# Optimization experiments

Measured on AMD Instinct MI355X. Metric: run time of the kernel, lower is better.

Reference implementation:

```python
import jax, jax.numpy as jnp
import numpy as np

N = 50000   # nodes
E = 800000  # edges (avg degree 16)
D = 128     # in_dim == hidden_dim


def setup_inputs() -> dict:
    key = jax.random.key(0)
    ks = jax.random.split(key, 8)
    x = jax.random.normal(ks[0], (N, D), dtype=jnp.float32)
    edge_index = jax.random.randint(ks[1], (2, E), 0, N, dtype=jnp.int32)
    s = 1.0 / np.sqrt(D)  # glorot-ish scale
    W0 = jax.random.normal(ks[2], (D, D), dtype=jnp.float32) * s
    W1 = jax.random.normal(ks[3], (D, D), dtype=jnp.float32) * s
    W2 = jax.random.normal(ks[4], (D, D), dtype=jnp.float32) * s
    b0 = jnp.zeros((D,), dtype=jnp.float32)
    b1 = jnp.zeros((D,), dtype=jnp.float32)
    b2 = jnp.zeros((D,), dtype=jnp.float32)
    return {"x": x, "edge_index": edge_index,
            "W0": W0, "b0": b0, "W1": W1, "b1": b1, "W2": W2, "b2": b2}


def reference(x, edge_index, W0, b0, W1, b1, W2, b2):
    # PyG GCNConv defaults: add self-loops, symmetric D^-1/2 (A+I) D^-1/2 norm,
    # linear transform first, bias added after aggregation.
    src, dst = edge_index[0], edge_index[1]
    loops = jnp.arange(N, dtype=src.dtype)
    src_f = jnp.concatenate([src, loops])  # [E+N]
    dst_f = jnp.concatenate([dst, loops])
    deg = jax.ops.segment_sum(jnp.ones_like(src_f, dtype=x.dtype), dst_f, num_segments=N)
    dinv = jnp.where(deg > 0, jax.lax.rsqrt(deg), 0.0)
    norm = dinv[src_f] * dinv[dst_f]  # [E+N]

    def gcn_layer(h, W, b):
        h = h @ W                                # [N, D]
        msg = h[src_f] * norm[:, None]           # [E+N, D] gather
        agg = jax.ops.segment_sum(msg, dst_f, num_segments=N)  # scatter-add
        return agg + b

    h = jax.nn.relu(gcn_layer(x, W0, b0))  # dropout p=0.0 is a no-op
    h = jax.nn.relu(gcn_layer(h, W1, b1))
    return gcn_layer(h, W2, b2)
```

## Files before the change

kernel.cpp:

```cpp
#include <hip/hip_runtime.h>
#include <hip/hip_fp16.h>

#define NN 50000
#define NPAD 50048
#define NE 800000
#define D 128
#define BPAD 136

typedef __attribute__((ext_vector_type(8))) short bf16x8;
typedef __attribute__((ext_vector_type(4))) float f32x4;

__device__ inline unsigned short f2bf(float f) {
    unsigned int b = __float_as_uint(f);
    return (unsigned short)((b + 0x7FFFu + ((b >> 16) & 1u)) >> 16);
}
__device__ inline float bf2f(unsigned short u) {
    return __uint_as_float(((unsigned int)u) << 16);
}


__global__ void k_degree(const int* __restrict__ dst, int* __restrict__ cnt,
                         int* __restrict__ rank) {
    int e = blockIdx.x * 256 + threadIdx.x;
    if (e < NE) {
        int d = dst[e];
        rank[e] = atomicAdd(&cnt[d], 1);
    }
}

__global__ void k_scan_block(const int* __restrict__ cnt, int* __restrict__ excl,
                             int* __restrict__ bsum) {
    __shared__ int sm[256];
    int t = threadIdx.x;
    int idx = blockIdx.x * 256 + t;
    int v = (idx < NN) ? cnt[idx] : 0;
    sm[t] = v;
    __syncthreads();
    for (int o = 1; o < 256; o <<= 1) {
        int u = (t >= o) ? sm[t - o] : 0;
        __syncthreads();
        sm[t] += u;
        __syncthreads();
    }
    if (idx < NN) excl[idx] = sm[t] - v;
    if (t == 255) bsum[blockIdx.x] = sm[255];
}

__global__ void k_scan_top(const int* __restrict__ bsum, int* __restrict__ boff) {
    __shared__ int sm[256];
    const int NB = (NN + 255) / 256;
    int t = threadIdx.x;
    int v = (t < NB) ? bsum[t] : 0;
    sm[t] = v;
    __syncthreads();
    for (int o = 1; o < 256; o <<= 1) {
        int u = (t >= o) ? sm[t - o] : 0;
        __syncthreads();
        sm[t] += u;
        __syncthreads();
    }
    if (t < NB) boff[t] = sm[t] - v;
}

__global__ void k_scan_add(int* __restrict__ rowptr, const int* __restrict__ boff,
                           const int* __restrict__ cnt, float* __restrict__ dinv) {
    int idx = blockIdx.x * 256 + threadIdx.x;
    if (idx < NN) {
        rowptr[idx] += boff[idx >> 8];
        dinv[idx] = rsqrtf((float)(cnt[idx] + 1));
    } else if (idx == NN) {
        rowptr[NN] = NE;
    }
}

__global__ void k_fill(const int* __restrict__ src, const int* __restrict__ dst,
                       const int* __restrict__ rowptr, const int* __restrict__ rank,
                       int* __restrict__ col) {
    int e = blockIdx.x * 256 + threadIdx.x;
    if (e < NE) {
        int d = dst[e];
        int pos = rowptr[d] + rank[e];
        __builtin_nontemporal_store(src[e], &col[pos]);
    }
}


__global__ void k_convW3(const float* __restrict__ W0, const float* __restrict__ W1,
                         const float* __restrict__ W2, unsigned short* __restrict__ Wh,
                         unsigned short* __restrict__ Wl) {
    int i = blockIdx.x * 256 + threadIdx.x;
    if (i >= 3 * D * D) return;
    int m = i / (D * D), r = i - m * (D * D);
    const float* W = (m == 0) ? W0 : ((m == 1) ? W1 : W2);
    int k = r >> 7, c = r & 127;
    float v = W[r];
    unsigned short h = f2bf(v);
    unsigned short l = f2bf(v - bf2f(h));
    Wh[(size_t)m * D * D + c * D + k] = h;
    Wl[(size_t)m * D * D + c * D + k] = l;
}


__device__ inline void gemm_store(f32x4 acc[2][4], const float* __restrict__ dinv,
                                  __half* __restrict__ C, int R0, int C0, int lr, int lg) {
    #pragma unroll
    for (int fr = 0; fr < 2; fr++) {
        int rb = R0 + fr * 16 + lg * 4;
        #pragma unroll
        for (int j = 0; j < 4; j++) {
            int r = rb + j;
            if (r < NN) {
                float s = dinv[r];
                #pragma unroll
                for (int fc = 0; fc < 4; fc++)
                    C[(size_t)r * D + C0 + fc * 16 + lr] =
                        __float2half_rn(acc[fr][fc][j] * s);
            }
        }
    }
}

__global__ __launch_bounds__(256, 3) void k_gemm_mfma(
        const unsigned short* __restrict__ Ah, const unsigned short* __restrict__ Al,
        const unsigned short* __restrict__ BhT, const unsigned short* __restrict__ BlT,
        const float* __restrict__ dinv, __half* __restrict__ C) {
    __shared__ short Bs_h[D * BPAD];
    int t = threadIdx.x;
    {
        int c = t >> 1;
        int k0 = (t & 1) * 64;
        const unsigned short* gh = BhT + c * D + k0;
        short* dh = Bs_h + c * BPAD + k0;
        #pragma unroll
        for (int i = 0; i < 8; i++)
            *(int4*)(dh + i * 8) = *(const int4*)(gh + i * 8);
    }
    __syncthreads();

    int w = t >> 6, ln = t & 63;
    int wr = w >> 1, wc = w & 1;
    int R0 = blockIdx.x * 64 + wr * 32;
    int C0 = wc * 64;
    int lr = ln & 15, lg = ln >> 4;

    f32x4 acc[2][4];
    #pragma unroll
    for (int a = 0; a < 2; a++)
        #pragma unroll
        for (int b = 0; b < 4; b++)
            acc[a][b] = (f32x4){0.f, 0.f, 0.f, 0.f};

    const unsigned short* Abh = Ah + (size_t)(R0 + lr) * D + lg * 8;
    const unsigned short* Abl = Al + (size_t)(R0 + lr) * D + lg * 8;

    #pragma unroll
    for (int ks = 0; ks < 4; ks++) {
        int ko = ks * 32;
        bf16x8 fa_h[2], fa_l[2], fb_h[4], fb_l[4];
        #pragma unroll
        for (int fr = 0; fr < 2; fr++) {
            fa_h[fr] = *(const bf16x8*)(Abh + fr * 16 * D + ko);
            fa_l[fr] = *(const bf16x8*)(Abl + fr * 16 * D + ko);
        }
        #pragma unroll
        for (int fc = 0; fc < 4; fc++) {
            int ccol = C0 + fc * 16 + lr;
            fb_h[fc] = *(const bf16x8*)(Bs_h + ccol * BPAD + ko + lg * 8);
            fb_l[fc] = *(const bf16x8*)(BlT + (size_t)ccol * D + ko + lg * 8);
        }
        #pragma unroll
        for (int fr = 0; fr < 2; fr++) {
            #pragma unroll
            for (int fc = 0; fc < 4; fc++) {
                acc[fr][fc] = __builtin_amdgcn_mfma_f32_16x16x32_bf16(
                    fa_h[fr], fb_h[fc], acc[fr][fc], 0, 0, 0);
                acc[fr][fc] = __builtin_amdgcn_mfma_f32_16x16x32_bf16(
                    fa_l[fr], fb_h[fc], acc[fr][fc], 0, 0, 0);
                acc[fr][fc] = __builtin_amdgcn_mfma_f32_16x16x32_bf16(
                    fa_h[fr], fb_l[fc], acc[fr][fc], 0, 0, 0);
            }
        }
    }
    gemm_store(acc, dinv, C, R0, C0, lr, lg);
}

__global__ __launch_bounds__(256, 2) void k_gemm_mfma_x(
        const float* __restrict__ X,
        const unsigned short* __restrict__ BhT, const unsigned short* __restrict__ BlT,
        const float* __restrict__ dinv, __half* __restrict__ C) {
    __shared__ short Bs_h[D * BPAD];
    int t = threadIdx.x;
    {
        int c = t >> 1;
        int k0 = (t & 1) * 64;
        const unsigned short* gh = BhT + c * D + k0;
        short* dh = Bs_h + c * BPAD + k0;
        #pragma unroll
        for (int i = 0; i < 8; i++)
            *(int4*)(dh + i * 8) = *(const int4*)(gh + i * 8);
    }
    __syncthreads();

    int w = t >> 6, ln = t & 63;
    int wr = w >> 1, wc = w & 1;
    int R0 = blockIdx.x * 64 + wr * 32;
    int C0 = wc * 64;
    int lr = ln & 15, lg = ln >> 4;

    f32x4 acc[2][4];
    #pragma unroll
    for (int a = 0; a < 2; a++)
        #pragma unroll
        for (int b = 0; b < 4; b++)
            acc[a][b] = (f32x4){0.f, 0.f, 0.f, 0.f};

    const float* Ab = X + (size_t)(R0 + lr) * D + lg * 8;

    #pragma unroll
    for (int ks = 0; ks < 4; ks++) {
        int ko = ks * 32;
        bf16x8 fa_h[2], fa_l[2], fb_h[4], fb_l[4];
        #pragma unroll
        for (int fr = 0; fr < 2; fr++) {
            float4 p0 = *(const float4*)(Ab + fr * 16 * D + ko);
            float4 p1 = *(const float4*)(Ab + fr * 16 * D + ko + 4);
            float vv[8] = {p0.x, p0.y, p0.z, p0.w, p1.x, p1.y, p1.z, p1.w};
            #pragma unroll
            for (int j = 0; j < 8; j++) {
                unsigned short h = f2bf(vv[j]);
                fa_h[fr][j] = (short)h;
                fa_l[fr][j] = (short)f2bf(vv[j] - bf2f(h));
            }
        }
        #pragma unroll
        for (int fc = 0; fc < 4; fc++) {
            int ccol = C0 + fc * 16 + lr;
            fb_h[fc] = *(const bf16x8*)(Bs_h + ccol * BPAD + ko + lg * 8);
            fb_l[fc] = *(const bf16x8*)(BlT + (size_t)ccol * D + ko + lg * 8);
        }
        #pragma unroll
        for (int fr = 0; fr < 2; fr++) {
            #pragma unroll
            for (int fc = 0; fc < 4; fc++) {
                acc[fr][fc] = __builtin_amdgcn_mfma_f32_16x16x32_bf16(
                    fa_h[fr], fb_h[fc], acc[fr][fc], 0, 0, 0);
                acc[fr][fc] = __builtin_amdgcn_mfma_f32_16x16x32_bf16(
                    fa_l[fr], fb_h[fc], acc[fr][fc], 0, 0, 0);
                acc[fr][fc] = __builtin_amdgcn_mfma_f32_16x16x32_bf16(
                    fa_h[fr], fb_l[fc], acc[fr][fc], 0, 0, 0);
            }
        }
    }
    gemm_store(acc, dinv, C, R0, C0, lr, lg);
}


__global__ __launch_bounds__(256) void k_agg(const __half* __restrict__ T,
                                             const int* __restrict__ rowptr,
                                             const int* __restrict__ col,
                                             const float* __restrict__ dinv,
                                             const float* __restrict__ bias,
                                             unsigned short* __restrict__ Oh,
                                             unsigned short* __restrict__ Ol,
                                             float* __restrict__ Of, int mode) {
    int i = blockIdx.x * 8 + (threadIdx.x >> 5);
    int sl = threadIdx.x & 31;
    int f = sl * 4;
    float di = dinv[i];
    float2 raw = *(const float2*)(T + (size_t)i * D + f);
    __half2 s0 = *(__half2*)&raw.x, s1 = *(__half2*)&raw.y;
    float2 g0 = __half22float2(s0), g1 = __half22float2(s1);
    float a0 = g0.x, a1 = g0.y, a2 = g1.x, a3 = g1.y;

    int e = rowptr[i], r1 = rowptr[i + 1];
    for (; e + 8 <= r1; e += 8) {
        float2 rv[8];
        #pragma unroll
        for (int u = 0; u < 8; u++) {
            int s = col[e + u];
            rv[u] = *(const float2*)(T + (size_t)s * D + f);
        }
        #pragma unroll
        for (int u = 0; u < 8; u++) {
            __half2 x0 = *(__half2*)&rv[u].x, x1 = *(__half2*)&rv[u].y;
            float2 q0 = __half22float2(x0), q1 = __half22float2(x1);
            a0 += q0.x; a1 += q0.y; a2 += q1.x; a3 += q1.y;
        }
    }
    for (; e + 4 <= r1; e += 4) {
        float2 rv[4];
        #pragma unroll
        for (int u = 0; u < 4; u++) {
            int s = col[e + u];
            rv[u] = *(const float2*)(T + (size_t)s * D + f);
        }
        #pragma unroll
        for (int u = 0; u < 4; u++) {
            __half2 x0 = *(__half2*)&rv[u].x, x1 = *(__half2*)&rv[u].y;
            float2 q0 = __half22float2(x0), q1 = __half22float2(x1);
            a0 += q0.x; a1 += q0.y; a2 += q1.x; a3 += q1.y;
        }
    }
    for (; e < r1; e++) {
        int s = col[e];
        float2 rv = *(const float2*)(T + (size_t)s * D + f);
        __half2 x0 = *(__half2*)&rv.x, x1 = *(__half2*)&rv.y;
        float2 q0 = __half22float2(x0), q1 = __half22float2(x1);
        a0 += q0.x; a1 += q0.y; a2 += q1.x; a3 += q1.y;
    }

    float4 bv = *(const float4*)(bias + f);
    a0 = a0 * di + bv.x;
    a1 = a1 * di + bv.y;
    a2 = a2 * di + bv.z;
    a3 = a3 * di + bv.w;
    if (mode) {
        a0 = fmaxf(a0, 0.f); a1 = fmaxf(a1, 0.f);
        a2 = fmaxf(a2, 0.f); a3 = fmaxf(a3, 0.f);
        unsigned short h0 = f2bf(a0), h1 = f2bf(a1), h2 = f2bf(a2), h3 = f2bf(a3);
        unsigned short l0 = f2bf(a0 - bf2f(h0)), l1 = f2bf(a1 - bf2f(h1));
        unsigned short l2 = f2bf(a2 - bf2f(h2)), l3 = f2bf(a3 - bf2f(h3));
        uint2 ph = make_uint2((unsigned)h0 | ((unsigned)h1 << 16),
                              (unsigned)h2 | ((unsigned)h3 << 16));
        uint2 pl = make_uint2((unsigned)l0 | ((unsigned)l1 << 16),
                              (unsigned)l2 | ((unsigned)l3 << 16));
        *(uint2*)(Oh + (size_t)i * D + f) = ph;
        *(uint2*)(Ol + (size_t)i * D + f) = pl;
    } else {
        *(float4*)(Of + (size_t)i * D + f) = make_float4(a0, a1, a2, a3);
    }
}


extern "C" void kernel_launch(void* const* d_in, const int* in_sizes, int n_in,
                              void* d_out, int out_size, void* d_ws, size_t ws_size,
                              hipStream_t stream) {
    const float* x  = (const float*)d_in[0];
    const int* edge = (const int*)d_in[1];
    const float* W0 = (const float*)d_in[2];
    const float* b0 = (const float*)d_in[3];
    const float* W1 = (const float*)d_in[4];
    const float* b1 = (const float*)d_in[5];
    const float* W2 = (const float*)d_in[6];
    const float* b2 = (const float*)d_in[7];
    const int* src = edge;
    const int* dst = edge + NE;
    float* out = (float*)d_out;

    char* ws = (char*)d_ws;
    size_t off = 0;
    auto alloc = [&](size_t bytes) {
        void* p = ws + off;
        off += (bytes + 255) & ~(size_t)255;
        return p;
    };
    int*   cnt    = (int*)alloc(NN * 4);
    int*   rowptr = (int*)alloc((NN + 1) * 4);
    float* dinv   = (float*)alloc(NN * 4);
    int*   bsum   = (int*)alloc(256 * 4);
    int*   boff   = (int*)alloc(256 * 4);
    int*   rank   = (int*)alloc((size_t)NE * 4);
    int*   col    = (int*)alloc((size_t)NE * 4);
    unsigned short* Wh = (unsigned short*)alloc(3 * D * D * 2);
    unsigned short* Wl = (unsigned short*)alloc(3 * D * D * 2);
    unsigned short* Xh = (unsigned short*)alloc((size_t)NPAD * D * 2);
    unsigned short* Xl = (unsigned short*)alloc((size_t)NPAD * D * 2);
    __half* T = (__half*)alloc((size_t)NPAD * D * 2);

    hipMemsetAsync(cnt, 0, NN * 4, stream);

    k_degree<<<(NE + 255) / 256, 256, 0, stream>>>(dst, cnt, rank);
    k_scan_block<<<(NN + 255) / 256, 256, 0, stream>>>(cnt, rowptr, bsum);
    k_scan_top<<<1, 256, 0, stream>>>(bsum, boff);
    k_scan_add<<<(NN + 256) / 256, 256, 0, stream>>>(rowptr, boff, cnt, dinv);
    k_fill<<<(NE + 255) / 256, 256, 0, stream>>>(src, dst, rowptr, rank, col);
    k_convW3<<<(3 * D * D + 255) / 256, 256, 0, stream>>>(W0, W1, W2, Wh, Wl);

    const int ggrid = (NN + 63) / 64;
    const int agrid = NN / 8;

    k_gemm_mfma_x<<<ggrid, 256, 0, stream>>>(x, Wh, Wl, dinv, T);
    k_agg<<<agrid, 256, 0, stream>>>(T, rowptr, col, dinv, b0, Xh, Xl, out, 1);
    k_gemm_mfma<<<ggrid, 256, 0, stream>>>(Xh, Xl, Wh + D * D, Wl + D * D, dinv, T);
    k_agg<<<agrid, 256, 0, stream>>>(T, rowptr, col, dinv, b1, Xh, Xl, out, 1);
    k_gemm_mfma<<<ggrid, 256, 0, stream>>>(Xh, Xl, Wh + 2 * D * D, Wl + 2 * D * D, dinv, T);
    k_agg<<<agrid, 256, 0, stream>>>(T, rowptr, col, dinv, b2, Xh, Xl, out, 0);
}
```

Baseline: 244.0 us.

## Fuse aggregation with next-layer GEMM via shared-memory split-bf16 tile

Each middle layer now runs one kernel: a block aggregates 64 nodes, applies bias and ReLU, splits the result into bf16 hi/lo parts in shared memory, then runs the MFMA GEMM straight from LDS. This removes the global write and re-read of the Xh/Xl intermediates and two kernel launches. In exchange, each block's gather phase and GEMM phase run back to back without overlap. The weights now come from global memory instead of LDS, and there are fewer, larger blocks for the irregular gather.

```diff
diff --git a/kernel.cpp b/kernel.cpp
--- a/kernel.cpp
+++ b/kernel.cpp
@@ -6,6 +6,7 @@
 #define NE 800000
 #define D 128
 #define BPAD 136
+#define APAD 136
 
 typedef __attribute__((ext_vector_type(8))) short bf16x8;
 typedef __attribute__((ext_vector_type(4))) float f32x4;
@@ -120,69 +121,6 @@
     }
 }
 
-__global__ __launch_bounds__(256, 3) void k_gemm_mfma(
-        const unsigned short* __restrict__ Ah, const unsigned short* __restrict__ Al,
-        const unsigned short* __restrict__ BhT, const unsigned short* __restrict__ BlT,
-        const float* __restrict__ dinv, __half* __restrict__ C) {
-    __shared__ short Bs_h[D * BPAD];
-    int t = threadIdx.x;
-    {
-        int c = t >> 1;
-        int k0 = (t & 1) * 64;
-        const unsigned short* gh = BhT + c * D + k0;
-        short* dh = Bs_h + c * BPAD + k0;
-        #pragma unroll
-        for (int i = 0; i < 8; i++)
-            *(int4*)(dh + i * 8) = *(const int4*)(gh + i * 8);
-    }
-    __syncthreads();
-
-    int w = t >> 6, ln = t & 63;
-    int wr = w >> 1, wc = w & 1;
-    int R0 = blockIdx.x * 64 + wr * 32;
-    int C0 = wc * 64;
-    int lr = ln & 15, lg = ln >> 4;
-
-    f32x4 acc[2][4];
-    #pragma unroll
-    for (int a = 0; a < 2; a++)
-        #pragma unroll
-        for (int b = 0; b < 4; b++)
-            acc[a][b] = (f32x4){0.f, 0.f, 0.f, 0.f};
-
-    const unsigned short* Abh = Ah + (size_t)(R0 + lr) * D + lg * 8;
-    const unsigned short* Abl = Al + (size_t)(R0 + lr) * D + lg * 8;
-
-    #pragma unroll
-    for (int ks = 0; ks < 4; ks++) {
-        int ko = ks * 32;
-        bf16x8 fa_h[2], fa_l[2], fb_h[4], fb_l[4];
-        #pragma unroll
-        for (int fr = 0; fr < 2; fr++) {
-            fa_h[fr] = *(const bf16x8*)(Abh + fr * 16 * D + ko);
-            fa_l[fr] = *(const bf16x8*)(Abl + fr * 16 * D + ko);
-        }
-        #pragma unroll
-        for (int fc = 0; fc < 4; fc++) {
-            int ccol = C0 + fc * 16 + lr;
-            fb_h[fc] = *(const bf16x8*)(Bs_h + ccol * BPAD + ko + lg * 8);
-            fb_l[fc] = *(const bf16x8*)(BlT + (size_t)ccol * D + ko + lg * 8);
-        }
-        #pragma unroll
-        for (int fr = 0; fr < 2; fr++) {
-            #pragma unroll
-            for (int fc = 0; fc < 4; fc++) {
-                acc[fr][fc] = __builtin_amdgcn_mfma_f32_16x16x32_bf16(
-                    fa_h[fr], fb_h[fc], acc[fr][fc], 0, 0, 0);
-                acc[fr][fc] = __builtin_amdgcn_mfma_f32_16x16x32_bf16(
-                    fa_l[fr], fb_h[fc], acc[fr][fc], 0, 0, 0);
-                acc[fr][fc] = __builtin_amdgcn_mfma_f32_16x16x32_bf16(
-                    fa_h[fr], fb_l[fc], acc[fr][fc], 0, 0, 0);
-            }
-        }
-    }
-    gemm_store(acc, dinv, C, R0, C0, lr, lg);
-}
 
 __global__ __launch_bounds__(256, 2) void k_gemm_mfma_x(
         const float* __restrict__ X,
@@ -255,14 +193,124 @@
 }
 
 
-__global__ __launch_bounds__(256) void k_agg(const __half* __restrict__ T,
-                                             const int* __restrict__ rowptr,
-                                             const int* __restrict__ col,
-                                             const float* __restrict__ dinv,
-                                             const float* __restrict__ bias,
-                                             unsigned short* __restrict__ Oh,
-                                             unsigned short* __restrict__ Ol,
-                                             float* __restrict__ Of, int mode) {
+__global__ __launch_bounds__(256, 3) void k_agg_gemm(
+        const __half* __restrict__ T_in,
+        const int* __restrict__ rowptr, const int* __restrict__ col,
+        const float* __restrict__ dinv, const float* __restrict__ bias,
+        const unsigned short* __restrict__ BhT, const unsigned short* __restrict__ BlT,
+        __half* __restrict__ T_out) {
+    __shared__ short Ah_s[64 * APAD];
+    __shared__ short Al_s[64 * APAD];
+    int t = threadIdx.x;
+    int base = blockIdx.x * 64;
+    int g = t >> 5, sl = t & 31;
+    int f = sl * 4;
+
+    float4 bv = *(const float4*)(bias + f);
+
+    for (int j = 0; j < 8; j++) {
+        int n = g + j * 8;
+        int i = base + n;
+        float a0 = 0.f, a1 = 0.f, a2 = 0.f, a3 = 0.f;
+        if (i < NN) {
+            float di = dinv[i];
+            float2 raw = *(const float2*)(T_in + (size_t)i * D + f);
+            {
+                __half2 x0 = *(__half2*)&raw.x, x1 = *(__half2*)&raw.y;
+                float2 q0 = __half22float2(x0), q1 = __half22float2(x1);
+                a0 = q0.x; a1 = q0.y; a2 = q1.x; a3 = q1.y;
+            }
+            int e = rowptr[i], r1 = rowptr[i + 1];
+            for (; e + 8 <= r1; e += 8) {
+                float2 rv[8];
+                #pragma unroll
+                for (int u = 0; u < 8; u++) {
+                    int s = col[e + u];
+                    rv[u] = *(const float2*)(T_in + (size_t)s * D + f);
+                }
+                #pragma unroll
+                for (int u = 0; u < 8; u++) {
+                    __half2 x0 = *(__half2*)&rv[u].x, x1 = *(__half2*)&rv[u].y;
+                    float2 q0 = __half22float2(x0), q1 = __half22float2(x1);
+                    a0 += q0.x; a1 += q0.y; a2 += q1.x; a3 += q1.y;
+                }
+            }
+            for (; e < r1; e++) {
+                int s = col[e];
+                float2 rv = *(const float2*)(T_in + (size_t)s * D + f);
+                __half2 x0 = *(__half2*)&rv.x, x1 = *(__half2*)&rv.y;
+                float2 q0 = __half22float2(x0), q1 = __half22float2(x1);
+                a0 += q0.x; a1 += q0.y; a2 += q1.x; a3 += q1.y;
+            }
+            a0 = fmaxf(a0 * di + bv.x, 0.f);
+            a1 = fmaxf(a1 * di + bv.y, 0.f);
+            a2 = fmaxf(a2 * di + bv.z, 0.f);
+            a3 = fmaxf(a3 * di + bv.w, 0.f);
+        }
+        unsigned short h0 = f2bf(a0), h1 = f2bf(a1), h2 = f2bf(a2), h3 = f2bf(a3);
+        unsigned short l0 = f2bf(a0 - bf2f(h0)), l1 = f2bf(a1 - bf2f(h1));
+        unsigned short l2 = f2bf(a2 - bf2f(h2)), l3 = f2bf(a3 - bf2f(h3));
+        *(uint2*)(Ah_s + n * APAD + f) = make_uint2(
+            (unsigned)h0 | ((unsigned)h1 << 16), (unsigned)h2 | ((unsigned)h3 << 16));
+        *(uint2*)(Al_s + n * APAD + f) = make_uint2(
+            (unsigned)l0 | ((unsigned)l1 << 16), (unsigned)l2 | ((unsigned)l3 << 16));
+    }
+    __syncthreads();
+
+    int w = t >> 6, ln = t & 63;
+    int wr = w >> 1, wc = w & 1;
+    int R0 = base + wr * 32;
+    int C0 = wc * 64;
+    int lr = ln & 15, lg = ln >> 4;
+
+    f32x4 acc[2][4];
+    #pragma unroll
+    for (int a = 0; a < 2; a++)
+        #pragma unroll
+        for (int b = 0; b < 4; b++)
+            acc[a][b] = (f32x4){0.f, 0.f, 0.f, 0.f};
+
+    const short* As_h = Ah_s + (wr * 32 + lr) * APAD + lg * 8;
+    const short* As_l = Al_s + (wr * 32 + lr) * APAD + lg * 8;
+
+    #pragma unroll
+    for (int ks = 0; ks < 4; ks++) {
+        int ko = ks * 32;
+        bf16x8 fa_h[2], fa_l[2], fb_h[4], fb_l[4];
+        #pragma unroll
+        for (int fr = 0; fr < 2; fr++) {
+            fa_h[fr] = *(const bf16x8*)(As_h + fr * 16 * APAD + ko);
+            fa_l[fr] = *(const bf16x8*)(As_l + fr * 16 * APAD + ko);
+        }
+        #pragma unroll
+        for (int fc = 0; fc < 4; fc++) {
+            int ccol = C0 + fc * 16 + lr;
+            fb_h[fc] = *(const bf16x8*)(BhT + (size_t)ccol * D + ko + lg * 8);
+            fb_l[fc] = *(const bf16x8*)(BlT + (size_t)ccol * D + ko + lg * 8);
+        }
+        #pragma unroll
+        for (int fr = 0; fr < 2; fr++) {
+            #pragma unroll
+            for (int fc = 0; fc < 4; fc++) {
+                acc[fr][fc] = __builtin_amdgcn_mfma_f32_16x16x32_bf16(
+                    fa_h[fr], fb_h[fc], acc[fr][fc], 0, 0, 0);
+                acc[fr][fc] = __builtin_amdgcn_mfma_f32_16x16x32_bf16(
+                    fa_l[fr], fb_h[fc], acc[fr][fc], 0, 0, 0);
+                acc[fr][fc] = __builtin_amdgcn_mfma_f32_16x16x32_bf16(
+                    fa_h[fr], fb_l[fc], acc[fr][fc], 0, 0, 0);
+            }
+        }
+    }
+    gemm_store(acc, dinv, T_out, R0, C0, lr, lg);
+}
+
+
+__global__ __launch_bounds__(256) void k_agg_out(const __half* __restrict__ T,
+                                                 const int* __restrict__ rowptr,
+                                                 const int* __restrict__ col,
+                                                 const float* __restrict__ dinv,
+                                                 const float* __restrict__ bias,
+                                                 float* __restrict__ Of) {
     int i = blockIdx.x * 8 + (threadIdx.x >> 5);
     int sl = threadIdx.x & 31;
     int f = sl * 4;
@@ -287,20 +335,6 @@
             a0 += q0.x; a1 += q0.y; a2 += q1.x; a3 += q1.y;
         }
     }
-    for (; e + 4 <= r1; e += 4) {
-        float2 rv[4];
-        #pragma unroll
-        for (int u = 0; u < 4; u++) {
-            int s = col[e + u];
-            rv[u] = *(const float2*)(T + (size_t)s * D + f);
-        }
-        #pragma unroll
-        for (int u = 0; u < 4; u++) {
-            __half2 x0 = *(__half2*)&rv[u].x, x1 = *(__half2*)&rv[u].y;
-            float2 q0 = __half22float2(x0), q1 = __half22float2(x1);
-            a0 += q0.x; a1 += q0.y; a2 += q1.x; a3 += q1.y;
-        }
-    }
     for (; e < r1; e++) {
         int s = col[e];
         float2 rv = *(const float2*)(T + (size_t)s * D + f);
@@ -310,25 +344,8 @@
     }
 
     float4 bv = *(const float4*)(bias + f);
-    a0 = a0 * di + bv.x;
-    a1 = a1 * di + bv.y;
-    a2 = a2 * di + bv.z;
-    a3 = a3 * di + bv.w;
-    if (mode) {
-        a0 = fmaxf(a0, 0.f); a1 = fmaxf(a1, 0.f);
-        a2 = fmaxf(a2, 0.f); a3 = fmaxf(a3, 0.f);
-        unsigned short h0 = f2bf(a0), h1 = f2bf(a1), h2 = f2bf(a2), h3 = f2bf(a3);
-        unsigned short l0 = f2bf(a0 - bf2f(h0)), l1 = f2bf(a1 - bf2f(h1));
-        unsigned short l2 = f2bf(a2 - bf2f(h2)), l3 = f2bf(a3 - bf2f(h3));
-        uint2 ph = make_uint2((unsigned)h0 | ((unsigned)h1 << 16),
-                              (unsigned)h2 | ((unsigned)h3 << 16));
-        uint2 pl = make_uint2((unsigned)l0 | ((unsigned)l1 << 16),
-                              (unsigned)l2 | ((unsigned)l3 << 16));
-        *(uint2*)(Oh + (size_t)i * D + f) = ph;
-        *(uint2*)(Ol + (size_t)i * D + f) = pl;
-    } else {
-        *(float4*)(Of + (size_t)i * D + f) = make_float4(a0, a1, a2, a3);
-    }
+    *(float4*)(Of + (size_t)i * D + f) = make_float4(
+        a0 * di + bv.x, a1 * di + bv.y, a2 * di + bv.z, a3 * di + bv.w);
 }
 
 
@@ -363,9 +380,8 @@
     int*   col    = (int*)alloc((size_t)NE * 4);
     unsigned short* Wh = (unsigned short*)alloc(3 * D * D * 2);
     unsigned short* Wl = (unsigned short*)alloc(3 * D * D * 2);
-    unsigned short* Xh = (unsigned short*)alloc((size_t)NPAD * D * 2);
-    unsigned short* Xl = (unsigned short*)alloc((size_t)NPAD * D * 2);
-    __half* T = (__half*)alloc((size_t)NPAD * D * 2);
+    __half* Ta = (__half*)alloc((size_t)NPAD * D * 2);
+    __half* Tb = (__half*)alloc((size_t)NPAD * D * 2);
 
     hipMemsetAsync(cnt, 0, NN * 4, stream);
 
@@ -379,10 +395,10 @@
     const int ggrid = (NN + 63) / 64;
     const int agrid = NN / 8;
 
-    k_gemm_mfma_x<<<ggrid, 256, 0, stream>>>(x, Wh, Wl, dinv, T);
-    k_agg<<<agrid, 256, 0, stream>>>(T, rowptr, col, dinv, b0, Xh, Xl, out, 1);
-    k_gemm_mfma<<<ggrid, 256, 0, stream>>>(Xh, Xl, Wh + D * D, Wl + D * D, dinv, T);
-    k_agg<<<agrid, 256, 0, stream>>>(T, rowptr, col, dinv, b1, Xh, Xl, out, 1);
-    k_gemm_mfma<<<ggrid, 256, 0, stream>>>(Xh, Xl, Wh + 2 * D * D, Wl + 2 * D * D, dinv, T);
-    k_agg<<<agrid, 256, 0, stream>>>(T, rowptr, col, dinv, b2, Xh, Xl, out, 0);
-}
+    k_gemm_mfma_x<<<ggrid, 256, 0, stream>>>(x, Wh, Wl, dinv, Ta);
+    k_agg_gemm<<<ggrid, 256, 0, stream>>>(Ta, rowptr, col, dinv, b0,
+                                          Wh + D * D, Wl + D * D, Tb);
+    k_agg_gemm<<<ggrid, 256, 0, stream>>>(Tb, rowptr, col, dinv, b1,
+                                          Wh + 2 * D * D, Wl + 2 * D * D, Ta);
+    k_agg_out<<<agrid, 256, 0, stream>>>(Ta, rowptr, col, dinv, b2, out);
+}
```

After: 266.1 us. +9.1%, slower.

## Store hidden activations in fp16 and widen aggregation loads to 16 bytes

Applied to the files above, without the earlier changes.

The aggregation kernel now writes one fp16 hidden buffer instead of separate bf16 hi/lo planes, and the GEMM splits each fp16 value into bf16 hi/lo in registers. This halves activation write and read traffic between layers. Aggregation now uses 16 lanes per node with 8 features each, so every gather is a 16-byte load, and the 4-edge tail loop is dropped. The degree kernel also writes rank with a nontemporal store. Storing hidden activations in fp16 loses a little precision compared with the bf16 hi/lo pair.

```diff
diff --git a/kernel.cpp b/kernel.cpp
--- a/kernel.cpp
+++ b/kernel.cpp
@@ -24,7 +24,8 @@
     int e = blockIdx.x * 256 + threadIdx.x;
     if (e < NE) {
         int d = dst[e];
-        rank[e] = atomicAdd(&cnt[d], 1);
+        int r = atomicAdd(&cnt[d], 1);
+        __builtin_nontemporal_store(r, &rank[e]);
     }
 }
 
@@ -120,69 +121,6 @@
     }
 }
 
-__global__ __launch_bounds__(256, 3) void k_gemm_mfma(
-        const unsigned short* __restrict__ Ah, const unsigned short* __restrict__ Al,
-        const unsigned short* __restrict__ BhT, const unsigned short* __restrict__ BlT,
-        const float* __restrict__ dinv, __half* __restrict__ C) {
-    __shared__ short Bs_h[D * BPAD];
-    int t = threadIdx.x;
-    {
-        int c = t >> 1;
-        int k0 = (t & 1) * 64;
-        const unsigned short* gh = BhT + c * D + k0;
-        short* dh = Bs_h + c * BPAD + k0;
-        #pragma unroll
-        for (int i = 0; i < 8; i++)
-            *(int4*)(dh + i * 8) = *(const int4*)(gh + i * 8);
-    }
-    __syncthreads();
-
-    int w = t >> 6, ln = t & 63;
-    int wr = w >> 1, wc = w & 1;
-    int R0 = blockIdx.x * 64 + wr * 32;
-    int C0 = wc * 64;
-    int lr = ln & 15, lg = ln >> 4;
-
-    f32x4 acc[2][4];
-    #pragma unroll
-    for (int a = 0; a < 2; a++)
-        #pragma unroll
-        for (int b = 0; b < 4; b++)
-            acc[a][b] = (f32x4){0.f, 0.f, 0.f, 0.f};
-
-    const unsigned short* Abh = Ah + (size_t)(R0 + lr) * D + lg * 8;
-    const unsigned short* Abl = Al + (size_t)(R0 + lr) * D + lg * 8;
-
-    #pragma unroll
-    for (int ks = 0; ks < 4; ks++) {
-        int ko = ks * 32;
-        bf16x8 fa_h[2], fa_l[2], fb_h[4], fb_l[4];
-        #pragma unroll
-        for (int fr = 0; fr < 2; fr++) {
-            fa_h[fr] = *(const bf16x8*)(Abh + fr * 16 * D + ko);
-            fa_l[fr] = *(const bf16x8*)(Abl + fr * 16 * D + ko);
-        }
-        #pragma unroll
-        for (int fc = 0; fc < 4; fc++) {
-            int ccol = C0 + fc * 16 + lr;
-            fb_h[fc] = *(const bf16x8*)(Bs_h + ccol * BPAD + ko + lg * 8);
-            fb_l[fc] = *(const bf16x8*)(BlT + (size_t)ccol * D + ko + lg * 8);
-        }
-        #pragma unroll
-        for (int fr = 0; fr < 2; fr++) {
-            #pragma unroll
-            for (int fc = 0; fc < 4; fc++) {
-                acc[fr][fc] = __builtin_amdgcn_mfma_f32_16x16x32_bf16(
-                    fa_h[fr], fb_h[fc], acc[fr][fc], 0, 0, 0);
-                acc[fr][fc] = __builtin_amdgcn_mfma_f32_16x16x32_bf16(
-                    fa_l[fr], fb_h[fc], acc[fr][fc], 0, 0, 0);
-                acc[fr][fc] = __builtin_amdgcn_mfma_f32_16x16x32_bf16(
-                    fa_h[fr], fb_l[fc], acc[fr][fc], 0, 0, 0);
-            }
-        }
-    }
-    gemm_store(acc, dinv, C, R0, C0, lr, lg);
-}
 
 __global__ __launch_bounds__(256, 2) void k_gemm_mfma_x(
         const float* __restrict__ X,
@@ -255,80 +193,202 @@
 }
 
 
-__global__ __launch_bounds__(256) void k_agg(const __half* __restrict__ T,
-                                             const int* __restrict__ rowptr,
-                                             const int* __restrict__ col,
-                                             const float* __restrict__ dinv,
-                                             const float* __restrict__ bias,
-                                             unsigned short* __restrict__ Oh,
-                                             unsigned short* __restrict__ Ol,
-                                             float* __restrict__ Of, int mode) {
-    int i = blockIdx.x * 8 + (threadIdx.x >> 5);
-    int sl = threadIdx.x & 31;
-    int f = sl * 4;
+__global__ __launch_bounds__(256, 3) void k_gemm_mfma_h(
+        const __half* __restrict__ H,
+        const unsigned short* __restrict__ BhT, const unsigned short* __restrict__ BlT,
+        const float* __restrict__ dinv, __half* __restrict__ C) {
+    __shared__ short Bs_h[D * BPAD];
+    int t = threadIdx.x;
+    {
+        int c = t >> 1;
+        int k0 = (t & 1) * 64;
+        const unsigned short* gh = BhT + c * D + k0;
+        short* dh = Bs_h + c * BPAD + k0;
+        #pragma unroll
+        for (int i = 0; i < 8; i++)
+            *(int4*)(dh + i * 8) = *(const int4*)(gh + i * 8);
+    }
+    __syncthreads();
+
+    int w = t >> 6, ln = t & 63;
+    int wr = w >> 1, wc = w & 1;
+    int R0 = blockIdx.x * 64 + wr * 32;
+    int C0 = wc * 64;
+    int lr = ln & 15, lg = ln >> 4;
+
+    f32x4 acc[2][4];
+    #pragma unroll
+    for (int a = 0; a < 2; a++)
+        #pragma unroll
+        for (int b = 0; b < 4; b++)
+            acc[a][b] = (f32x4){0.f, 0.f, 0.f, 0.f};
+
+    const __half* Ab = H + (size_t)(R0 + lr) * D + lg * 8;
+
+    #pragma unroll
+    for (int ks = 0; ks < 4; ks++) {
+        int ko = ks * 32;
+        bf16x8 fa_h[2], fa_l[2], fb_h[4], fb_l[4];
+        #pragma unroll
+        for (int fr = 0; fr < 2; fr++) {
+            float4 p = *(const float4*)(Ab + fr * 16 * D + ko);
+            const __half2* hp = (const __half2*)&p;
+            #pragma unroll
+            for (int q = 0; q < 4; q++) {
+                float2 fv = __half22float2(hp[q]);
+                unsigned short h0 = f2bf(fv.x), h1 = f2bf(fv.y);
+                fa_h[fr][q * 2]     = (short)h0;
+                fa_h[fr][q * 2 + 1] = (short)h1;
+                fa_l[fr][q * 2]     = (short)f2bf(fv.x - bf2f(h0));
+                fa_l[fr][q * 2 + 1] = (short)f2bf(fv.y - bf2f(h1));
+            }
+        }
+        #pragma unroll
+        for (int fc = 0; fc < 4; fc++) {
+            int ccol = C0 + fc * 16 + lr;
+            fb_h[fc] = *(const bf16x8*)(Bs_h + ccol * BPAD + ko + lg * 8);
+            fb_l[fc] = *(const bf16x8*)(BlT + (size_t)ccol * D + ko + lg * 8);
+        }
+        #pragma unroll
+        for (int fr = 0; fr < 2; fr++) {
+            #pragma unroll
+            for (int fc = 0; fc < 4; fc++) {
+                acc[fr][fc] = __builtin_amdgcn_mfma_f32_16x16x32_bf16(
+                    fa_h[fr], fb_h[fc], acc[fr][fc], 0, 0, 0);
+                acc[fr][fc] = __builtin_amdgcn_mfma_f32_16x16x32_bf16(
+                    fa_l[fr], fb_h[fc], acc[fr][fc], 0, 0, 0);
+                acc[fr][fc] = __builtin_amdgcn_mfma_f32_16x16x32_bf16(
+                    fa_h[fr], fb_l[fc], acc[fr][fc], 0, 0, 0);
+            }
+        }
+    }
+    gemm_store(acc, dinv, C, R0, C0, lr, lg);
+}
+
+
+__global__ __launch_bounds__(256) void k_agg_relu(const __half* __restrict__ T,
+                                                  const int* __restrict__ rowptr,
+                                                  const int* __restrict__ col,
+                                                  const float* __restrict__ dinv,
+                                                  const float* __restrict__ bias,
+                                                  __half* __restrict__ Hout) {
+    int i = blockIdx.x * 16 + (threadIdx.x >> 4);
+    int sl = threadIdx.x & 15;
+    int f = sl * 8;
     float di = dinv[i];
-    float2 raw = *(const float2*)(T + (size_t)i * D + f);
-    __half2 s0 = *(__half2*)&raw.x, s1 = *(__half2*)&raw.y;
-    float2 g0 = __half22float2(s0), g1 = __half22float2(s1);
-    float a0 = g0.x, a1 = g0.y, a2 = g1.x, a3 = g1.y;
-
+    float a[8];
+    {
+        float4 raw = *(const float4*)(T + (size_t)i * D + f);
+        const __half2* hp = (const __half2*)&raw;
+        #pragma unroll
+        for (int q = 0; q < 4; q++) {
+            float2 fv = __half22float2(hp[q]);
+            a[q * 2] = fv.x;
+            a[q * 2 + 1] = fv.y;
+        }
+    }
     int e = rowptr[i], r1 = rowptr[i + 1];
     for (; e + 8 <= r1; e += 8) {
-        float2 rv[8];
+        float4 rv[8];
         #pragma unroll
         for (int u = 0; u < 8; u++) {
             int s = col[e + u];
-            rv[u] = *(const float2*)(T + (size_t)s * D + f);
+            rv[u] = *(const float4*)(T + (size_t)s * D + f);
         }
         #pragma unroll
         for (int u = 0; u < 8; u++) {
-            __half2 x0 = *(__half2*)&rv[u].x, x1 = *(__half2*)&rv[u].y;
-            float2 q0 = __half22float2(x0), q1 = __half22float2(x1);
-            a0 += q0.x; a1 += q0.y; a2 += q1.x; a3 += q1.y;
-        }
-    }
-    for (; e + 4 <= r1; e += 4) {
-        float2 rv[4];
-        #pragma unroll
-        for (int u = 0; u < 4; u++) {
-            int s = col[e + u];
-            rv[u] = *(const float2*)(T + (size_t)s * D + f);
-        }
-        #pragma unroll
-        for (int u = 0; u < 4; u++) {
-            __half2 x0 = *(__half2*)&rv[u].x, x1 = *(__half2*)&rv[u].y;
-            float2 q0 = __half22float2(x0), q1 = __half22float2(x1);
-            a0 += q0.x; a1 += q0.y; a2 += q1.x; a3 += q1.y;
+            const __half2* hp = (const __half2*)&rv[u];
+            #pragma unroll
+            for (int q = 0; q < 4; q++) {
+                float2 fv = __half22float2(hp[q]);
+                a[q * 2] += fv.x;
+                a[q * 2 + 1] += fv.y;
+            }
         }
     }
     for (; e < r1; e++) {
         int s = col[e];
-        float2 rv = *(const float2*)(T + (size_t)s * D + f);
-        __half2 x0 = *(__half2*)&rv.x, x1 = *(__half2*)&rv.y;
-        float2 q0 = __half22float2(x0), q1 = __half22float2(x1);
-        a0 += q0.x; a1 += q0.y; a2 += q1.x; a3 += q1.y;
-    }
-
-    float4 bv = *(const float4*)(bias + f);
-    a0 = a0 * di + bv.x;
-    a1 = a1 * di + bv.y;
-    a2 = a2 * di + bv.z;
-    a3 = a3 * di + bv.w;
-    if (mode) {
-        a0 = fmaxf(a0, 0.f); a1 = fmaxf(a1, 0.f);
-        a2 = fmaxf(a2, 0.f); a3 = fmaxf(a3, 0.f);
-        unsigned short h0 = f2bf(a0), h1 = f2bf(a1), h2 = f2bf(a2), h3 = f2bf(a3);
-        unsigned short l0 = f2bf(a0 - bf2f(h0)), l1 = f2bf(a1 - bf2f(h1));
-        unsigned short l2 = f2bf(a2 - bf2f(h2)), l3 = f2bf(a3 - bf2f(h3));
-        uint2 ph = make_uint2((unsigned)h0 | ((unsigned)h1 << 16),
-                              (unsigned)h2 | ((unsigned)h3 << 16));
-        uint2 pl = make_uint2((unsigned)l0 | ((unsigned)l1 << 16),
-                              (unsigned)l2 | ((unsigned)l3 << 16));
-        *(uint2*)(Oh + (size_t)i * D + f) = ph;
-        *(uint2*)(Ol + (size_t)i * D + f) = pl;
-    } else {
-        *(float4*)(Of + (size_t)i * D + f) = make_float4(a0, a1, a2, a3);
-    }
+        float4 rv = *(const float4*)(T + (size_t)s * D + f);
+        const __half2* hp = (const __half2*)&rv;
+        #pragma unroll
+        for (int q = 0; q < 4; q++) {
+            float2 fv = __half22float2(hp[q]);
+            a[q * 2] += fv.x;
+            a[q * 2 + 1] += fv.y;
+        }
+    }
+    float4 bv0 = *(const float4*)(bias + f);
+    float4 bv1 = *(const float4*)(bias + f + 4);
+    float bb[8] = {bv0.x, bv0.y, bv0.z, bv0.w, bv1.x, bv1.y, bv1.z, bv1.w};
+    __half2 o[4];
+    #pragma unroll
+    for (int q = 0; q < 4; q++) {
+        float x0 = fmaxf(a[q * 2] * di + bb[q * 2], 0.f);
+        float x1 = fmaxf(a[q * 2 + 1] * di + bb[q * 2 + 1], 0.f);
+        o[q] = __floats2half2_rn(x0, x1);
+    }
+    *(float4*)(Hout + (size_t)i * D + f) = *(float4*)o;
+}
+
+__global__ __launch_bounds__(256) void k_agg_out(const __half* __restrict__ T,
+                                                 const int* __restrict__ rowptr,
+                                                 const int* __restrict__ col,
+                                                 const float* __restrict__ dinv,
+                                                 const float* __restrict__ bias,
+                                                 float* __restrict__ Of) {
+    int i = blockIdx.x * 16 + (threadIdx.x >> 4);
+    int sl = threadIdx.x & 15;
+    int f = sl * 8;
+    float di = dinv[i];
+    float a[8];
+    {
+        float4 raw = *(const float4*)(T + (size_t)i * D + f);
+        const __half2* hp = (const __half2*)&raw;
+        #pragma unroll
+        for (int q = 0; q < 4; q++) {
+            float2 fv = __half22float2(hp[q]);
+            a[q * 2] = fv.x;
+            a[q * 2 + 1] = fv.y;
+        }
+    }
+    int e = rowptr[i], r1 = rowptr[i + 1];
+    for (; e + 8 <= r1; e += 8) {
+        float4 rv[8];
+        #pragma unroll
+        for (int u = 0; u < 8; u++) {
+            int s = col[e + u];
+            rv[u] = *(const float4*)(T + (size_t)s * D + f);
+        }
+        #pragma unroll
+        for (int u = 0; u < 8; u++) {
+            const __half2* hp = (const __half2*)&rv[u];
+            #pragma unroll
+            for (int q = 0; q < 4; q++) {
+                float2 fv = __half22float2(hp[q]);
+                a[q * 2] += fv.x;
+                a[q * 2 + 1] += fv.y;
+            }
+        }
+    }
+    for (; e < r1; e++) {
+        int s = col[e];
+        float4 rv = *(const float4*)(T + (size_t)s * D + f);
+        const __half2* hp = (const __half2*)&rv;
+        #pragma unroll
+        for (int q = 0; q < 4; q++) {
+            float2 fv = __half22float2(hp[q]);
+            a[q * 2] += fv.x;
+            a[q * 2 + 1] += fv.y;
+        }
+    }
+    float4 bv0 = *(const float4*)(bias + f);
+    float4 bv1 = *(const float4*)(bias + f + 4);
+    float4 o0 = make_float4(a[0] * di + bv0.x, a[1] * di + bv0.y,
+                            a[2] * di + bv0.z, a[3] * di + bv0.w);
+    float4 o1 = make_float4(a[4] * di + bv1.x, a[5] * di + bv1.y,
+                            a[6] * di + bv1.z, a[7] * di + bv1.w);
+    *(float4*)(Of + (size_t)i * D + f) = o0;
+    *(float4*)(Of + (size_t)i * D + f + 4) = o1;
 }
 
 
@@ -363,9 +423,9 @@
     int*   col    = (int*)alloc((size_t)NE * 4);
     unsigned short* Wh = (unsigned short*)alloc(3 * D * D * 2);
     unsigned short* Wl = (unsigned short*)alloc(3 * D * D * 2);
-    unsigned short* Xh = (unsigned short*)alloc((size_t)NPAD * D * 2);
-    unsigned short* Xl = (unsigned short*)alloc((size_t)NPAD * D * 2);
-    __half* T = (__half*)alloc((size_t)NPAD * D * 2);
+    __half* Ta = (__half*)alloc((size_t)NPAD * D * 2);
+    __half* Tb = (__half*)alloc((size_t)NPAD * D * 2);
+    __half* Hb = (__half*)alloc((size_t)NPAD * D * 2);
 
     hipMemsetAsync(cnt, 0, NN * 4, stream);
 
@@ -377,12 +437,12 @@
     k_convW3<<<(3 * D * D + 255) / 256, 256, 0, stream>>>(W0, W1, W2, Wh, Wl);
 
     const int ggrid = (NN + 63) / 64;
-    const int agrid = NN / 8;
-
-    k_gemm_mfma_x<<<ggrid, 256, 0, stream>>>(x, Wh, Wl, dinv, T);
-    k_agg<<<agrid, 256, 0, stream>>>(T, rowptr, col, dinv, b0, Xh, Xl, out, 1);
-    k_gemm_mfma<<<ggrid, 256, 0, stream>>>(Xh, Xl, Wh + D * D, Wl + D * D, dinv, T);
-    k_agg<<<agrid, 256, 0, stream>>>(T, rowptr, col, dinv, b1, Xh, Xl, out, 1);
-    k_gemm_mfma<<<ggrid, 256, 0, stream>>>(Xh, Xl, Wh + 2 * D * D, Wl + 2 * D * D, dinv, T);
-    k_agg<<<agrid, 256, 0, stream>>>(T, rowptr, col, dinv, b2, Xh, Xl, out, 0);
-}
+    const int agrid = NN / 16;
+
+    k_gemm_mfma_x<<<ggrid, 256, 0, stream>>>(x, Wh, Wl, dinv, Ta);
+    k_agg_relu<<<agrid, 256, 0, stream>>>(Ta, rowptr, col, dinv, b0, Hb);
+    k_gemm_mfma_h<<<ggrid, 256, 0, stream>>>(Hb, Wh + D * D, Wl + D * D, dinv, Tb);
+    k_agg_relu<<<agrid, 256, 0, stream>>>(Tb, rowptr, col, dinv, b1, Hb);
+    k_gemm_mfma_h<<<ggrid, 256, 0, stream>>>(Hb, Wh + 2 * D * D, Wl + 2 * D * D, dinv, Ta);
+    k_agg_out<<<agrid, 256, 0, stream>>>(Ta, rowptr, col, dinv, b2, out);
+}
```

Measured after the change: 243.6 us. About the same (-0.2%).
